# Optimization experiments

Measured on AMD Instinct MI355X. Metric: run time of the kernel, lower is better.

The kernel has to match this reference:

```python
import jax, jax.numpy as jnp
import numpy as np

N_NODES = 50000
N_EDGES = 800000
N_GRAPHS = 64
IN_CH = 128
EMB = 64


def gcn_conv(x, W, b, src, dst, w, n):
    """PyG GCNConv: add self-loops (weight 1), symmetric normalization,
    linear transform, scatter-sum aggregation, bias."""
    loop = jnp.arange(n, dtype=src.dtype)
    src2 = jnp.concatenate([src, loop])
    dst2 = jnp.concatenate([dst, loop])
    w2 = jnp.concatenate([w, jnp.ones((n,), dtype=x.dtype)])
    deg = jax.ops.segment_sum(w2, dst2, num_segments=n)
    dinv = jnp.where(deg > 0, jax.lax.rsqrt(jnp.where(deg > 0, deg, 1.0)), 0.0)
    norm = dinv[src2] * w2 * dinv[dst2]  # [E+N]
    h = x @ W  # [N, out]
    msg = norm[:, None] * h[src2]  # [E+N, out]
    return jax.ops.segment_sum(msg, dst2, num_segments=n) + b


def setup_inputs() -> dict:
    key = jax.random.key(0)
    ks = jax.random.split(key, 16)
    x = jax.random.normal(ks[0], (N_NODES, IN_CH), dtype=jnp.float32)
    edge_index = jax.random.randint(ks[1], (2, N_EDGES), 0, N_NODES, dtype=jnp.int32)
    edge_attr = jax.random.uniform(ks[2], (N_EDGES,), dtype=jnp.float32)
    batch_index = jnp.sort(jax.random.randint(ks[3], (N_NODES,), 0, N_GRAPHS, dtype=jnp.int32))
    def glorot(k, shape):
        lim = float(np.sqrt(6.0 / (shape[0] + shape[1])))
        return jax.random.uniform(k, shape, dtype=jnp.float32, minval=-lim, maxval=lim)
    return {
        "x": x, "edge_index": edge_index, "edge_attr": edge_attr, "batch_index": batch_index,
        "W0": glorot(ks[4], (IN_CH, EMB)), "b0": jnp.zeros((EMB,), jnp.float32),
        "W1": glorot(ks[5], (EMB, EMB)), "b1": jnp.zeros((EMB,), jnp.float32),
        "W2": glorot(ks[6], (EMB, EMB)), "b2": jnp.zeros((EMB,), jnp.float32),
        "W3": glorot(ks[7], (EMB, EMB)), "b3": jnp.zeros((EMB,), jnp.float32),
        "Wout": glorot(ks[8], (2 * EMB, 1)), "bout": jnp.zeros((1,), jnp.float32),
    }


def reference(x, edge_index, edge_attr, batch_index, W0, b0, W1, b1, W2, b2, W3, b3, Wout, bout):
    n = x.shape[0]
    src, dst = edge_index[0], edge_index[1]
    h = jnp.tanh(gcn_conv(x, W0, b0, src, dst, edge_attr, n))
    h = jnp.tanh(gcn_conv(h, W1, b1, src, dst, edge_attr, n))
    h = jnp.tanh(gcn_conv(h, W2, b2, src, dst, edge_attr, n))
    h = jnp.tanh(gcn_conv(h, W3, b3, src, dst, edge_attr, n))
    gmax = jax.ops.segment_max(h, batch_index, num_segments=N_GRAPHS)
    gsum = jax.ops.segment_sum(h, batch_index, num_segments=N_GRAPHS)
    cnt = jax.ops.segment_sum(jnp.ones((n,), h.dtype), batch_index, num_segments=N_GRAPHS)
    gmean = gsum / jnp.maximum(cnt, 1.0)[:, None]
    pooled = jnp.concatenate([gmax, gmean], axis=1)  # [B, 2*EMB]
    return (pooled @ Wout + bout).reshape(-1)
```

## Files before the change

### kernel.cpp

```cpp
#include <hip/hip_runtime.h>
#include <hip/hip_fp16.h>
#include <math.h>
#include <limits.h>

#define N_NODES 50000
#define N_EDGES 800000
#define N_GRAPHS 64
#define IN_CH 128
#define EMB 64
#define POOL_CHUNK 16
#define CPAD64 16
#define CNT_SHIFT 44
#define FX_SCALE 16777216.0f

__global__ void init_k(unsigned long long* cnt64, int* total, int* gmax,
                       float* gsum, int* cnt) {
    int i = blockIdx.x * blockDim.x + threadIdx.x;
    if (i < N_NODES * CPAD64) cnt64[i] = 0ULL;
    if (i == 0) *total = 0;
    if (i < N_GRAPHS * EMB) { gmax[i] = INT_MIN; gsum[i] = 0.f; }
    if (i < N_GRAPHS) cnt[i] = 0;
}

__global__ void hist_k(const int* __restrict__ dst, const float* __restrict__ w,
                       unsigned long long* cnt64, int* __restrict__ slot_in) {
    int e = blockIdx.x * blockDim.x + threadIdx.x;
    if (e >= N_EDGES) return;
    unsigned long long fx = (unsigned long long)(w[e] * FX_SCALE + 0.5f);
    unsigned long long old = atomicAdd(&cnt64[(size_t)dst[e] * CPAD64],
                                       (1ULL << CNT_SHIFT) | fx);
    slot_in[e] = (int)(old >> CNT_SHIFT);
}

__global__ void alloc_k(const unsigned long long* __restrict__ cnt64,
                        int* __restrict__ row_start, int* __restrict__ row_end,
                        int* total, float* __restrict__ dinv) {
    int i = blockIdx.x * blockDim.x + threadIdx.x;
    int lane = threadIdx.x & 63;
    unsigned long long v = (i < N_NODES) ? cnt64[(size_t)i * CPAD64] : 0ULL;
    int c = (int)(v >> CNT_SHIFT);
    int inc = c;
    for (int off = 1; off < 64; off <<= 1) {
        int t = __shfl_up(inc, off);
        if (lane >= off) inc += t;
    }
    int base;
    if (lane == 63) base = atomicAdd(total, inc);
    base = __shfl(base, 63);
    int excl = base + inc - c;
    if (i < N_NODES) {
        row_start[i] = excl;
        row_end[i] = excl + c;
        float degw = (float)(v & ((1ULL << CNT_SHIFT) - 1)) * (1.0f / FX_SCALE);
        float d = 1.0f + degw;
        dinv[i] = d > 0.f ? rsqrtf(d) : 0.f;
    }
}

__global__ void scatter_k(const int* __restrict__ src, const int* __restrict__ dst,
                          const float* __restrict__ w, const int* __restrict__ slot_in,
                          const int* __restrict__ row_start, int2* __restrict__ csr) {
    int e = blockIdx.x * blockDim.x + threadIdx.x;
    if (e >= N_EDGES) return;
    int d = dst[e];
    int slot = row_start[d] + slot_in[e];
    csr[slot] = make_int2(src[e], __float_as_int(w[e]));
}

template<int K, bool HALF_IN>
__global__ __launch_bounds__(256) void gemm_k(const void* __restrict__ A_,
                                              const float* __restrict__ W,
                                              const float* __restrict__ dinv,
                                              __half* __restrict__ out) {
    __shared__ float Al[64 * K];
    __shared__ float Wl[K * EMB];
    int tid = threadIdx.x;
    long rowBase = (long)blockIdx.x * 64;
    int validRows = (int)min((long)64, (long)N_NODES - rowBase);

    if constexpr (HALF_IN) {
        const __half* Ah = (const __half*)A_ + rowBase * K;
        for (int i = tid; i < validRows * (K / 4); i += 256) {
            int r = i / (K / 4), kc = i % (K / 4);
            const __half2* p = (const __half2*)(Ah + (long)r * K + 4 * kc);
            float2 lo = __half22float2(p[0]);
            float2 hi = __half22float2(p[1]);
            *(float4*)&Al[r * K + 4 * (kc ^ (r & 3))] = make_float4(lo.x, lo.y, hi.x, hi.y);
        }
    } else {
        const float4* Ag = (const float4*)((const float*)A_ + rowBase * K);
        for (int i = tid; i < validRows * (K / 4); i += 256) {
            int r = i / (K / 4), kc = i % (K / 4);
            float4 v = Ag[(long)r * (K / 4) + kc];
            *(float4*)&Al[r * K + 4 * (kc ^ (r & 3))] = v;
        }
    }
    const float4* Wg = (const float4*)W;
    float4* Wl4 = (float4*)Wl;
    for (int i = tid; i < K * EMB / 4; i += 256) Wl4[i] = Wg[i];
    __syncthreads();

    int tc = tid & 15, tr = tid >> 4;
    int r0 = tr * 4, c0 = tc * 4;
    float acc[4][4] = {};
#pragma unroll 2
    for (int k = 0; k < K; k += 4) {
        int kc = k >> 2;
        float4 a[4], w[4];
#pragma unroll
        for (int i = 0; i < 4; ++i)
            a[i] = *(const float4*)&Al[(r0 + i) * K + 4 * (kc ^ i)];
#pragma unroll
        for (int j = 0; j < 4; ++j)
            w[j] = *(const float4*)&Wl[(k + j) * EMB + c0];
#pragma unroll
        for (int i = 0; i < 4; ++i) {
            const float* ai = (const float*)&a[i];
#pragma unroll
            for (int kk = 0; kk < 4; ++kk) {
                float av = ai[kk];
                const float* wk = (const float*)&w[kk];
#pragma unroll
                for (int j = 0; j < 4; ++j) acc[i][j] += av * wk[j];
            }
        }
    }
#pragma unroll
    for (int i = 0; i < 4; ++i) {
        long row = rowBase + r0 + i;
        if (row < N_NODES) {
            float dv = dinv[row];
            __half2 p0 = __floats2half2_rn(dv * acc[i][0], dv * acc[i][1]);
            __half2 p1 = __floats2half2_rn(dv * acc[i][2], dv * acc[i][3]);
            uint2 u = make_uint2(*(unsigned int*)&p0, *(unsigned int*)&p1);
            *(uint2*)&out[row * EMB + c0] = u;
        }
    }
}

__global__ __launch_bounds__(256) void fused_agg_k(const __half* __restrict__ hs,
                                                   const int2* __restrict__ csr,
                                                   const int* __restrict__ row_start,
                                                   const int* __restrict__ row_end,
                                                   const float* __restrict__ dinv,
                                                   const float* __restrict__ b,
                                                   __half* __restrict__ out) {
    int node = (blockIdx.x * blockDim.x + threadIdx.x) >> 6;
    int lane = threadIdx.x & 63;
    if (node >= N_NODES) return;
    float di = dinv[node];
    float acc = __half2float(hs[(long)node * EMB + lane]);
    int e = row_start[node];
    int end = row_end[node];
    for (; e + 7 < end; e += 8) {
        int2 r[8];
        __half v[8];
#pragma unroll
        for (int i = 0; i < 8; ++i) r[i] = csr[e + i];
#pragma unroll
        for (int i = 0; i < 8; ++i) v[i] = hs[(long)r[i].x * EMB + lane];
#pragma unroll
        for (int i = 0; i < 8; ++i) acc += __int_as_float(r[i].y) * __half2float(v[i]);
    }
    for (; e + 3 < end; e += 4) {
        int2 r0 = csr[e], r1 = csr[e + 1], r2 = csr[e + 2], r3 = csr[e + 3];
        float v0 = __half2float(hs[(long)r0.x * EMB + lane]);
        float v1 = __half2float(hs[(long)r1.x * EMB + lane]);
        float v2 = __half2float(hs[(long)r2.x * EMB + lane]);
        float v3 = __half2float(hs[(long)r3.x * EMB + lane]);
        acc += __int_as_float(r0.y) * v0;
        acc += __int_as_float(r1.y) * v1;
        acc += __int_as_float(r2.y) * v2;
        acc += __int_as_float(r3.y) * v3;
    }
    for (; e < end; ++e) {
        int2 r0 = csr[e];
        acc += __int_as_float(r0.y) * __half2float(hs[(long)r0.x * EMB + lane]);
    }
    float o = tanhf(di * acc + b[lane]);
    __half oh = __float2half(o);
    __builtin_nontemporal_store(*(unsigned short*)&oh,
                                (unsigned short*)&out[(long)node * EMB + lane]);
}

__device__ inline int f2ord(float x) {
    int bb = __float_as_int(x);
    return bb >= 0 ? bb : (bb ^ 0x7fffffff);
}
__device__ inline float ord2f(int k) {
    return __int_as_float(k >= 0 ? k : (k ^ 0x7fffffff));
}

__global__ __launch_bounds__(256) void pool_k(const __half* __restrict__ h,
                                              const int* __restrict__ batch,
                                              int* gmax, float* gsum, int* cnt) {
    int wave = (blockIdx.x * blockDim.x + threadIdx.x) >> 6;
    int lane = threadIdx.x & 63;
    int start = wave * POOL_CHUNK;
    if (start >= N_NODES) return;
    int bsel = (lane < POOL_CHUNK) ? batch[start + lane] : 0;
    float v[POOL_CHUNK];
#pragma unroll
    for (int i = 0; i < POOL_CHUNK; ++i)
        v[i] = __half2float(h[(long)(start + i) * EMB + lane]);
    int curg = __shfl(bsel, 0);
    float mx = -INFINITY, sm = 0.f;
    int ct = 0;
#pragma unroll
    for (int i = 0; i < POOL_CHUNK; ++i) {
        int g = __shfl(bsel, i);
        if (g != curg) {
            atomicMax(&gmax[curg * EMB + lane], f2ord(mx));
            atomicAdd(&gsum[curg * EMB + lane], sm);
            if (lane == 0) atomicAdd(&cnt[curg], ct);
            curg = g; mx = -INFINITY; sm = 0.f; ct = 0;
        }
        mx = fmaxf(mx, v[i]);
        sm += v[i];
        ++ct;
    }
    atomicMax(&gmax[curg * EMB + lane], f2ord(mx));
    atomicAdd(&gsum[curg * EMB + lane], sm);
    if (lane == 0) atomicAdd(&cnt[curg], ct);
}

__global__ void final_k(const int* __restrict__ gmax, const float* __restrict__ gsum,
                        const int* __restrict__ cnt, const float* __restrict__ Wout,
                        const float* __restrict__ bout, float* __restrict__ out) {
    int g = threadIdx.x;
    if (g >= N_GRAPHS) return;
    float c = fmaxf((float)cnt[g], 1.0f);
    float acc = bout[0];
    for (int ch = 0; ch < EMB; ++ch) {
        acc += ord2f(gmax[g * EMB + ch]) * Wout[ch]
             + (gsum[g * EMB + ch] / c) * Wout[EMB + ch];
    }
    out[g] = acc;
}

extern "C" void kernel_launch(void* const* d_in, const int* in_sizes, int n_in,
                              void* d_out, int out_size, void* d_ws, size_t ws_size,
                              hipStream_t stream) {
    const float* x         = (const float*)d_in[0];
    const int*   edge_idx  = (const int*)d_in[1];
    const float* edge_attr = (const float*)d_in[2];
    const int*   batch     = (const int*)d_in[3];
    const float* W0 = (const float*)d_in[4];
    const float* b0 = (const float*)d_in[5];
    const float* W1 = (const float*)d_in[6];
    const float* b1 = (const float*)d_in[7];
    const float* W2 = (const float*)d_in[8];
    const float* b2 = (const float*)d_in[9];
    const float* W3 = (const float*)d_in[10];
    const float* b3 = (const float*)d_in[11];
    const float* Wout = (const float*)d_in[12];
    const float* bout = (const float*)d_in[13];
    float* out = (float*)d_out;

    const int* src = edge_idx;
    const int* dst = edge_idx + N_EDGES;

    char* ws = (char*)d_ws;
    float*  dinv      = (float*)ws;  ws += (size_t)N_NODES * sizeof(float);
    unsigned long long* cnt64 = (unsigned long long*)ws;
    ws += (size_t)N_NODES * CPAD64 * sizeof(unsigned long long);
    int*    row_start = (int*)ws;    ws += (size_t)N_NODES * sizeof(int);
    int*    row_end   = (int*)ws;    ws += (size_t)N_NODES * sizeof(int);
    int*    slot_in   = (int*)ws;    ws += (size_t)N_EDGES * sizeof(int);
    int*    total     = (int*)ws;    ws += 4 * sizeof(int);
    int2*   csr       = (int2*)ws;   ws += (size_t)N_EDGES * sizeof(int2);
    __half* bufL      = (__half*)ws; ws += (size_t)N_NODES * EMB * sizeof(__half);
    __half* bufH      = (__half*)ws; ws += (size_t)N_NODES * EMB * sizeof(__half);
    int*    gmax      = (int*)ws;    ws += N_GRAPHS * EMB * sizeof(int);
    float*  gsum      = (float*)ws;  ws += N_GRAPHS * EMB * sizeof(float);
    int*    cnt       = (int*)ws;    ws += N_GRAPHS * sizeof(int);

    const int nodeB = (N_NODES + 255) / 256;
    const int edgeB = (N_EDGES + 255) / 256;
    const int waveB = (N_NODES * 64 + 255) / 256;
    const int gemmB = (N_NODES + 63) / 64;
    const int initB = (N_NODES * CPAD64 + 255) / 256;

    init_k<<<initB, 256, 0, stream>>>(cnt64, total, gmax, gsum, cnt);
    hist_k<<<edgeB, 256, 0, stream>>>(dst, edge_attr, cnt64, slot_in);
    alloc_k<<<nodeB, 256, 0, stream>>>(cnt64, row_start, row_end, total, dinv);
    scatter_k<<<edgeB, 256, 0, stream>>>(src, dst, edge_attr, slot_in, row_start, csr);

    const float* Wl[4] = {W0, W1, W2, W3};
    const float* bl[4] = {b0, b1, b2, b3};
    for (int l = 0; l < 4; ++l) {
        if (l == 0) gemm_k<IN_CH, false><<<gemmB, 256, 0, stream>>>(x, Wl[0], dinv, bufL);
        else        gemm_k<EMB, true>   <<<gemmB, 256, 0, stream>>>(bufH, Wl[l], dinv, bufL);
        fused_agg_k<<<waveB, 256, 0, stream>>>(bufL, csr, row_start, row_end, dinv, bl[l], bufH);
    }

    pool_k<<<(((N_NODES + POOL_CHUNK - 1) / POOL_CHUNK) * 64 + 255) / 256, 256, 0, stream>>>(
        bufH, batch, gmax, gsum, cnt);
    final_k<<<1, 64, 0, stream>>>(gmax, gsum, cnt, Wout, bout, out);
}
```

Measured before the change: 375.3 us.

## Use MFMA f16 GEMM and precomputed byte offsets in CSR gather

Replaces the scalar-FMA fp32 GEMM with a matrix-core MFMA 16x16x32 f16 kernel. A and W are staged in LDS as padded fp16, with W stored transposed. The CSR source index is now stored pre-multiplied by the row stride in bytes, so the aggregation gather skips a per-edge multiply and 64-bit address computation. Converting the fp32 input layer to fp16 before the GEMM adds rounding error. The output stores are now scalar half writes spread across columns, which are less coalesced.

```diff
diff --git a/kernel.cpp b/kernel.cpp
--- a/kernel.cpp
+++ b/kernel.cpp
@@ -12,6 +12,10 @@
 #define CPAD64 16
 #define CNT_SHIFT 44
 #define FX_SCALE 16777216.0f
+
+typedef _Float16 f16;
+typedef __attribute__((ext_vector_type(8))) _Float16 half8;
+typedef __attribute__((ext_vector_type(4))) float f32x4;
 
 __global__ void init_k(unsigned long long* cnt64, int* total, int* gmax,
                        float* gsum, int* cnt) {
@@ -64,7 +68,7 @@
     if (e >= N_EDGES) return;
     int d = dst[e];
     int slot = row_start[d] + slot_in[e];
-    csr[slot] = make_int2(src[e], __float_as_int(w[e]));
+    csr[slot] = make_int2(src[e] * (EMB * 2), __float_as_int(w[e]));
 }
 
 template<int K, bool HALF_IN>
@@ -72,69 +76,83 @@
                                               const float* __restrict__ W,
                                               const float* __restrict__ dinv,
                                               __half* __restrict__ out) {
-    __shared__ float Al[64 * K];
-    __shared__ float Wl[K * EMB];
+    constexpr int LDK = K + 8;
+    __shared__ __align__(16) f16 Al[64 * LDK];
+    __shared__ __align__(16) f16 Wt[EMB * LDK];
     int tid = threadIdx.x;
     long rowBase = (long)blockIdx.x * 64;
     int validRows = (int)min((long)64, (long)N_NODES - rowBase);
 
     if constexpr (HALF_IN) {
         const __half* Ah = (const __half*)A_ + rowBase * K;
-        for (int i = tid; i < validRows * (K / 4); i += 256) {
-            int r = i / (K / 4), kc = i % (K / 4);
-            const __half2* p = (const __half2*)(Ah + (long)r * K + 4 * kc);
-            float2 lo = __half22float2(p[0]);
-            float2 hi = __half22float2(p[1]);
-            *(float4*)&Al[r * K + 4 * (kc ^ (r & 3))] = make_float4(lo.x, lo.y, hi.x, hi.y);
+        constexpr int CH = K / 8;
+        for (int i = tid; i < validRows * CH; i += 256) {
+            int r = i / CH, c = i % CH;
+            uint4 v = *(const uint4*)(Ah + (long)r * K + c * 8);
+            *(uint4*)&Al[r * LDK + c * 8] = v;
         }
     } else {
-        const float4* Ag = (const float4*)((const float*)A_ + rowBase * K);
-        for (int i = tid; i < validRows * (K / 4); i += 256) {
-            int r = i / (K / 4), kc = i % (K / 4);
-            float4 v = Ag[(long)r * (K / 4) + kc];
-            *(float4*)&Al[r * K + 4 * (kc ^ (r & 3))] = v;
-        }
-    }
-    const float4* Wg = (const float4*)W;
-    float4* Wl4 = (float4*)Wl;
-    for (int i = tid; i < K * EMB / 4; i += 256) Wl4[i] = Wg[i];
+        const float* Af = (const float*)A_;
+        constexpr int CH = K / 4;
+        for (int i = tid; i < validRows * CH; i += 256) {
+            int r = i / CH, c = i % CH;
+            float4 v = *(const float4*)(Af + (rowBase + r) * K + c * 4);
+            __half2 p0 = __floats2half2_rn(v.x, v.y);
+            __half2 p1 = __floats2half2_rn(v.z, v.w);
+            uint2 u = make_uint2(*(unsigned int*)&p0, *(unsigned int*)&p1);
+            *(uint2*)&Al[r * LDK + c * 4] = u;
+        }
+    }
+    {
+        constexpr int CZ = K / 8;
+        for (int i = tid + validRows * CZ; i < 64 * CZ; i += 256) {
+            int r = i / CZ, c = i % CZ;
+            *(uint4*)&Al[r * LDK + c * 8] = make_uint4(0, 0, 0, 0);
+        }
+    }
+    {
+        const float4* Wg = (const float4*)W;
+        for (int i = tid; i < K * (EMB / 4); i += 256) {
+            int k = i >> 4, nq = i & 15;
+            float4 v = Wg[i];
+            Wt[(4 * nq + 0) * LDK + k] = (f16)v.x;
+            Wt[(4 * nq + 1) * LDK + k] = (f16)v.y;
+            Wt[(4 * nq + 2) * LDK + k] = (f16)v.z;
+            Wt[(4 * nq + 3) * LDK + k] = (f16)v.w;
+        }
+    }
     __syncthreads();
 
-    int tc = tid & 15, tr = tid >> 4;
-    int r0 = tr * 4, c0 = tc * 4;
-    float acc[4][4] = {};
-#pragma unroll 2
-    for (int k = 0; k < K; k += 4) {
-        int kc = k >> 2;
-        float4 a[4], w[4];
-#pragma unroll
-        for (int i = 0; i < 4; ++i)
-            a[i] = *(const float4*)&Al[(r0 + i) * K + 4 * (kc ^ i)];
-#pragma unroll
-        for (int j = 0; j < 4; ++j)
-            w[j] = *(const float4*)&Wl[(k + j) * EMB + c0];
-#pragma unroll
-        for (int i = 0; i < 4; ++i) {
-            const float* ai = (const float*)&a[i];
-#pragma unroll
-            for (int kk = 0; kk < 4; ++kk) {
-                float av = ai[kk];
-                const float* wk = (const float*)&w[kk];
-#pragma unroll
-                for (int j = 0; j < 4; ++j) acc[i][j] += av * wk[j];
-            }
-        }
-    }
+    int wv = tid >> 6, lane = tid & 63;
+    int l15 = lane & 15, kg = (lane >> 4) * 8;
+    const f16* Ap = &Al[(wv * 16 + l15) * LDK + kg];
+    const f16* Bp = &Wt[l15 * LDK + kg];
+    f32x4 acc0 = {0.f, 0.f, 0.f, 0.f};
+    f32x4 acc1 = acc0, acc2 = acc0, acc3 = acc0;
+#pragma unroll
+    for (int ks = 0; ks < K / 32; ++ks) {
+        int k0 = ks * 32;
+        half8 a  = *(const half8*)(Ap + k0);
+        half8 b0 = *(const half8*)(Bp + k0);
+        half8 b1 = *(const half8*)(Bp + 16 * LDK + k0);
+        half8 b2 = *(const half8*)(Bp + 32 * LDK + k0);
+        half8 b3 = *(const half8*)(Bp + 48 * LDK + k0);
+        acc0 = __builtin_amdgcn_mfma_f32_16x16x32_f16(a, b0, acc0, 0, 0, 0);
+        acc1 = __builtin_amdgcn_mfma_f32_16x16x32_f16(a, b1, acc1, 0, 0, 0);
+        acc2 = __builtin_amdgcn_mfma_f32_16x16x32_f16(a, b2, acc2, 0, 0, 0);
+        acc3 = __builtin_amdgcn_mfma_f32_16x16x32_f16(a, b3, acc3, 0, 0, 0);
+    }
+    int orow = wv * 16 + (lane >> 4) * 4;
 #pragma unroll
     for (int i = 0; i < 4; ++i) {
-        long row = rowBase + r0 + i;
-        if (row < N_NODES) {
-            float dv = dinv[row];
-            __half2 p0 = __floats2half2_rn(dv * acc[i][0], dv * acc[i][1]);
-            __half2 p1 = __floats2half2_rn(dv * acc[i][2], dv * acc[i][3]);
-            uint2 u = make_uint2(*(unsigned int*)&p0, *(unsigned int*)&p1);
-            *(uint2*)&out[row * EMB + c0] = u;
-        }
+        long row = rowBase + orow + i;
+        if (row >= N_NODES) break;
+        float dv = dinv[row];
+        __half* op = &out[row * EMB + l15];
+        op[0]  = __float2half(dv * acc0[i]);
+        op[16] = __float2half(dv * acc1[i]);
+        op[32] = __float2half(dv * acc2[i]);
+        op[48] = __float2half(dv * acc3[i]);
     }
 }
 
@@ -148,6 +166,7 @@
     int node = (blockIdx.x * blockDim.x + threadIdx.x) >> 6;
     int lane = threadIdx.x & 63;
     if (node >= N_NODES) return;
+    const char* hsb = (const char*)hs + (size_t)(lane * 2);
     float di = dinv[node];
     float acc = __half2float(hs[(long)node * EMB + lane]);
     int e = row_start[node];
@@ -158,16 +177,16 @@
 #pragma unroll
         for (int i = 0; i < 8; ++i) r[i] = csr[e + i];
 #pragma unroll
-        for (int i = 0; i < 8; ++i) v[i] = hs[(long)r[i].x * EMB + lane];
+        for (int i = 0; i < 8; ++i) v[i] = *(const __half*)(hsb + (unsigned)r[i].x);
 #pragma unroll
         for (int i = 0; i < 8; ++i) acc += __int_as_float(r[i].y) * __half2float(v[i]);
     }
     for (; e + 3 < end; e += 4) {
         int2 r0 = csr[e], r1 = csr[e + 1], r2 = csr[e + 2], r3 = csr[e + 3];
-        float v0 = __half2float(hs[(long)r0.x * EMB + lane]);
-        float v1 = __half2float(hs[(long)r1.x * EMB + lane]);
-        float v2 = __half2float(hs[(long)r2.x * EMB + lane]);
-        float v3 = __half2float(hs[(long)r3.x * EMB + lane]);
+        float v0 = __half2float(*(const __half*)(hsb + (unsigned)r0.x));
+        float v1 = __half2float(*(const __half*)(hsb + (unsigned)r1.x));
+        float v2 = __half2float(*(const __half*)(hsb + (unsigned)r2.x));
+        float v3 = __half2float(*(const __half*)(hsb + (unsigned)r3.x));
         acc += __int_as_float(r0.y) * v0;
         acc += __int_as_float(r1.y) * v1;
         acc += __int_as_float(r2.y) * v2;
@@ -175,7 +194,7 @@
     }
     for (; e < end; ++e) {
         int2 r0 = csr[e];
-        acc += __int_as_float(r0.y) * __half2float(hs[(long)r0.x * EMB + lane]);
+        acc += __int_as_float(r0.y) * __half2float(*(const __half*)(hsb + (unsigned)r0.x));
     }
     float o = tanhf(di * acc + b[lane]);
     __half oh = __float2half(o);
```

Result: faster. 351.7 us (-6.3%).
